# Performance work log

Measured on AMD Instinct MI355X. Metric: run time of the kernel, lower is better.

Reference implementation:

```python
import jax, jax.numpy as jnp
import numpy as np

GAMMA = 0.1   # sdtw_gamma from train_config
WARP = 1.0    # sdtw_warp from train_config
BIG = 1e8     # stand-in for +inf in the DP table (safe in fp32 logsumexp)


def soft_dtw(D, gamma, warp):
    """SoftDTW with warp penalty via anti-diagonal wavefront DP.

    D: [B, N, M] pairwise cost matrix. Returns [B] soft-DTW values.
    Recurrence: R[i,j] = D[i,j] + softmin_gamma(R[i-1,j-1], R[i-1,j]+warp, R[i,j-1]+warp)
    """
    B, N, M = D.shape
    R = jnp.full((B, N + 1, M + 1), BIG, D.dtype)
    R = R.at[:, 0, 0].set(0.0)
    ii = jnp.arange(N)  # cell row indices on a diagonal

    def body(R, k):
        jj = k - ii                       # cell col indices, i+j = k
        valid = (jj >= 0) & (jj < M)
        jc = jnp.clip(jj, 0, M - 1)
        # padded-coordinate predecessors of cell (ii, jj)
        r_diag = R[:, ii, jc]             # R[i-1, j-1]
        r_up = R[:, ii, jc + 1] + warp    # R[i-1, j] + warp
        r_left = R[:, ii + 1, jc] + warp  # R[i, j-1] + warp
        stacked = jnp.stack([r_diag, r_up, r_left], axis=0)  # [3, B, N]
        smin = -gamma * jax.nn.logsumexp(-stacked / gamma, axis=0)
        new = D[:, ii, jc] + smin
        cur = R[:, ii + 1, jc + 1]
        upd = jnp.where(valid[None, :], new, cur)
        # row indices ii+1 are all distinct -> no scatter collisions
        R = R.at[:, ii + 1, jc + 1].set(upd)
        return R, None

    R, _ = jax.lax.scan(body, R, jnp.arange(N + M - 1))
    return R[:, N, M]


def setup_inputs() -> dict:
    key = jax.random.key(0)
    k1, k2, k3, k4 = jax.random.split(key, 4)
    mel_pred = jax.random.normal(k1, (4, 512, 80), dtype=jnp.float32)
    mel_target = jax.random.normal(k2, (4, 512, 80), dtype=jnp.float32)
    log_d_pred = jax.random.normal(k3, (4, 128), dtype=jnp.float32)
    d_target = jax.random.randint(k4, (4, 128), 0, 20)
    return {"mel_pred": mel_pred, "mel_target": mel_target,
            "log_d_pred": log_d_pred, "d_target": d_target}


def reference(mel_pred, mel_target, log_d_pred, d_target):
    B, T, _ = mel_pred.shape
    # pairwise L1 frame distance: D[b,i,j] = sum_m |pred[b,i,m] - tgt[b,j,m]|
    D = jnp.abs(mel_pred[:, :, None, :] - mel_target[:, None, :, :]).sum(-1)
    sdtw = soft_dtw(D, GAMMA, WARP)           # [B]
    mel_loss = (sdtw / T).mean()
    # L1 (reduction='none' -> mean) on log-durations
    log_d_target = jnp.log(d_target.astype(jnp.float32) + 1.0)
    duration_loss = jnp.abs(log_d_pred - log_d_target).mean()
    return mel_loss + duration_loss
```

## Files before the change

kernel.cpp:

```cpp
#include <hip/hip_runtime.h>
#include <hip/hip_bf16.h>
#include <hip/hip_fp16.h>
#include <math.h>

#define BIGF 1e8f
#define BIGS 28672.0f

__device__ inline float min3f(float a, float b, float c) {
    float d;
    asm("v_min3_f32 %0, %1, %2, %3" : "=v"(d) : "v"(a), "v"(b), "v"(c));
    return d;
}
__device__ inline float addh_lo(unsigned pw, float c) {
    float d;
    asm("v_fma_mix_f32 %0, %1, 1.0, %2 op_sel:[0,0,0] op_sel_hi:[1,0,0]"
        : "=v"(d) : "v"(pw), "v"(c));
    return d;
}
__device__ inline float addh_hi(unsigned pw, float c) {
    float d;
    asm("v_fma_mix_f32 %0, %1, 1.0, %2 op_sel:[1,0,0] op_sel_hi:[1,0,0]"
        : "=v"(d) : "v"(pw), "v"(c));
    return d;
}

__global__ __launch_bounds__(256) void prep_kernel(
        const float* __restrict__ pred, const float* __restrict__ targ,
        __half* __restrict__ Dh) {
    const int bid = blockIdx.x;
    const int t   = threadIdx.x;

    if (bid < 256) {
        const int b  = bid >> 6;
        const int i0 = ((bid >> 3) & 7) * 64;
        const int j0 = (bid & 7) * 64;
        __shared__ float sp[64][81];
        __shared__ float st[64][81];

        const float4* __restrict__ p4 = (const float4*)(pred + ((size_t)b * 512 + i0) * 80);
        const float4* __restrict__ t4 = (const float4*)(targ + ((size_t)b * 512 + j0) * 80);
        #pragma unroll
        for (int q = 0; q < 5; ++q) {
            int idx = q * 256 + t;
            int r = idx / 20, dq = idx % 20;
            float4 v = p4[r * 20 + dq];
            sp[r][dq*4+0]=v.x; sp[r][dq*4+1]=v.y; sp[r][dq*4+2]=v.z; sp[r][dq*4+3]=v.w;
            float4 w = t4[r * 20 + dq];
            st[r][dq*4+0]=w.x; st[r][dq*4+1]=w.y; st[r][dq*4+2]=w.z; st[r][dq*4+3]=w.w;
        }
        __syncthreads();

        const int tx = t & 15, ty = t >> 4;
        float acc[4][4];
        #pragma unroll
        for (int r = 0; r < 4; ++r)
            #pragma unroll
            for (int c = 0; c < 4; ++c) acc[r][c] = 0.f;

        #pragma unroll 4
        for (int d = 0; d < 80; ++d) {
            float a0 = sp[4*ty+0][d], a1 = sp[4*ty+1][d], a2 = sp[4*ty+2][d], a3 = sp[4*ty+3][d];
            float b0 = st[4*tx+0][d], b1 = st[4*tx+1][d], b2 = st[4*tx+2][d], b3 = st[4*tx+3][d];
            acc[0][0] += fabsf(a0-b0); acc[0][1] += fabsf(a0-b1); acc[0][2] += fabsf(a0-b2); acc[0][3] += fabsf(a0-b3);
            acc[1][0] += fabsf(a1-b0); acc[1][1] += fabsf(a1-b1); acc[1][2] += fabsf(a1-b2); acc[1][3] += fabsf(a1-b3);
            acc[2][0] += fabsf(a2-b0); acc[2][1] += fabsf(a2-b1); acc[2][2] += fabsf(a2-b2); acc[2][3] += fabsf(a2-b3);
            acc[3][0] += fabsf(a3-b0); acc[3][1] += fabsf(a3-b1); acc[3][2] += fabsf(a3-b2); acc[3][3] += fabsf(a3-b3);
        }

        #pragma unroll
        for (int r = 0; r < 4; ++r) {
            #pragma unroll
            for (int c = 0; c < 4; ++c) {
                int i = i0 + 4*ty + r;
                int j = j0 + 4*tx + c;
                float v = acc[r][c];
                float w = ((i | j) == 0) ? v : (v + 2.0f);
                Dh[((size_t)b * 1023 + (i + j)) * 512 + i] = __float2half(w);
            }
        }
    } else {
        const int k  = bid - 256;
        const int lo = (k > 511) ? (k - 511) : 0;
        const int hi = (k < 511) ? k : 511;
        const __half big = __float2half(BIGS);
        #pragma unroll
        for (int b = 0; b < 4; ++b) {
            __half* row = Dh + ((size_t)b * 1023 + k) * 512;
            int i1 = t;
            int i2 = t + 256;
            if (i1 < lo || i1 > hi) row[i1] = big;
            if (i2 < lo || i2 > hi) row[i2] = big;
        }
    }
}

#define DPPSHR(x) __int_as_float(__builtin_amdgcn_update_dpp(                 \
        __float_as_int(BIGF), __float_as_int(x), 0x138, 0xF, 0xF, false))

#define STEP(V1, V2, Q)                                                       \
  {                                                                           \
    float nb1 = DPPSHR(V1[7]);                                                \
    float nb2 = DPPSHR(V2[7]);                                                \
    V2[7] = addh_hi(Q.w, min3f(V2[6], V1[6], V1[7]));                         \
    V2[6] = addh_lo(Q.w, min3f(V2[5], V1[5], V1[6]));                         \
    V2[5] = addh_hi(Q.z, min3f(V2[4], V1[4], V1[5]));                         \
    V2[4] = addh_lo(Q.z, min3f(V2[3], V1[3], V1[4]));                         \
    V2[3] = addh_hi(Q.y, min3f(V2[2], V1[2], V1[3]));                         \
    V2[2] = addh_lo(Q.y, min3f(V2[1], V1[1], V1[2]));                         \
    V2[1] = addh_hi(Q.x, min3f(V2[0], V1[0], V1[1]));                         \
    V2[0] = addh_lo(Q.x, min3f(nb2,   nb1,   V1[0]));                         \
  }

__global__ __launch_bounds__(128, 1) void dp_kernel(
        const __half* __restrict__ Dh,
        const float* __restrict__ ldp, const int* __restrict__ dt,
        float* __restrict__ out) {
    const int tid = threadIdx.x;
    if (tid >= 64) {
        if (blockIdx.x == 0) {
            const int l = tid - 64;
            float s = 0.f;
            #pragma unroll
            for (int q = 0; q < 8; ++q) {
                int idx = l * 8 + q;
                s += fabsf(ldp[idx] - logf((float)dt[idx] + 1.0f));
            }
            #pragma unroll
            for (int o = 32; o > 0; o >>= 1) s += __shfl_down(s, o);
            if (l == 0) atomicAdd(out, s * (1.0f / 512.0f));
        }
        return;
    }

    const int b    = blockIdx.x;
    const int lane = tid;
    const char* __restrict__ base = (const char*)(Dh + (size_t)b * 1023 * 512);

    float A[8], B[8];
    #pragma unroll
    for (int r = 0; r < 8; ++r) { A[r] = BIGF; B[r] = BIGF; }

    {
        float c00 = __half2float(*(const __half*)base);
        B[0] = (lane == 0) ? c00 : BIGF;
    }
    __builtin_amdgcn_sched_barrier(0);

    unsigned voff = (unsigned)lane * 16u + 1024u;
    uint4 P[32];
    #pragma unroll
    for (int p = 0; p < 32; ++p) {
        asm volatile("global_load_dwordx4 %0, %1, %2"
                     : "=v"(P[p]) : "v"(voff), "s"(base) : "memory");
        voff += 1024u;
    }

    for (int t = 0; t < 31; ++t) {
#define PH(p, Vx, Vy)                                                         \
        asm volatile("s_waitcnt vmcnt(31)" ::: "memory");                     \
        __builtin_amdgcn_sched_barrier(0);                                    \
        STEP(Vx, Vy, P[p])                                                    \
        asm volatile("global_load_dwordx4 %0, %1, %2"                         \
                     : "=v"(P[p]) : "v"(voff), "s"(base) : "memory");         \
        voff += 1024u;
        PH(0,B,A)   PH(1,A,B)   PH(2,B,A)   PH(3,A,B)
        PH(4,B,A)   PH(5,A,B)   PH(6,B,A)   PH(7,A,B)
        PH(8,B,A)   PH(9,A,B)   PH(10,B,A)  PH(11,A,B)
        PH(12,B,A)  PH(13,A,B)  PH(14,B,A)  PH(15,A,B)
        PH(16,B,A)  PH(17,A,B)  PH(18,B,A)  PH(19,A,B)
        PH(20,B,A)  PH(21,A,B)  PH(22,B,A)  PH(23,A,B)
        PH(24,B,A)  PH(25,A,B)  PH(26,B,A)  PH(27,A,B)
        PH(28,B,A)  PH(29,A,B)  PH(30,B,A)  PH(31,A,B)
#undef PH
    }

    asm volatile("s_waitcnt vmcnt(0)" ::: "memory");
    __builtin_amdgcn_sched_barrier(0);
    STEP(B,A,P[0])   STEP(A,B,P[1])   STEP(B,A,P[2])   STEP(A,B,P[3])
    STEP(B,A,P[4])   STEP(A,B,P[5])   STEP(B,A,P[6])   STEP(A,B,P[7])
    STEP(B,A,P[8])   STEP(A,B,P[9])   STEP(B,A,P[10])  STEP(A,B,P[11])
    STEP(B,A,P[12])  STEP(A,B,P[13])  STEP(B,A,P[14])  STEP(A,B,P[15])
    STEP(B,A,P[16])  STEP(A,B,P[17])  STEP(B,A,P[18])  STEP(A,B,P[19])
    STEP(B,A,P[20])  STEP(A,B,P[21])  STEP(B,A,P[22])  STEP(A,B,P[23])
    STEP(B,A,P[24])  STEP(A,B,P[25])  STEP(B,A,P[26])  STEP(A,B,P[27])
    STEP(B,A,P[28])  STEP(A,B,P[29])

    if (lane == 63) atomicAdd(out, (B[7] - 1022.0f) * (1.0f / 2048.0f));
}

extern "C" void kernel_launch(void* const* d_in, const int* in_sizes, int n_in,
                              void* d_out, int out_size, void* d_ws, size_t ws_size,
                              hipStream_t stream) {
    const float* pred = (const float*)d_in[0];
    const float* targ = (const float*)d_in[1];
    const float* ldp  = (const float*)d_in[2];
    const int*   dt   = (const int*)d_in[3];
    float* out = (float*)d_out;

    __half* Dh = (__half*)d_ws;

    hipMemsetAsync(out, 0, sizeof(float), stream);
    prep_kernel<<<256 + 1023, 256, 0, stream>>>(pred, targ, Dh);
    dp_kernel<<<4, 128, 0, stream>>>(Dh, ldp, dt, out);
}
```

Baseline: 73.12 us.

## Stream DP cost diagonals through LDS with global_load_lds ring buffer

Replaces the 32-register prefetch ring of global loads in the DP kernel with direct global-to-LDS DMA into a 32-slot shared-memory ring. Values are read back from LDS four steps ahead into a small set of registers. The goal is to free VGPRs and cut register pressure while keeping the deep prefetch that hides memory latency on the serial wavefront loop. It adds LDS read latency and relies on vmcnt accounting for the LDS DMA, which is delicate to get right.

```diff
diff --git a/kernel.cpp b/kernel.cpp
--- a/kernel.cpp
+++ b/kernel.cpp
@@ -22,6 +22,12 @@
     asm("v_fma_mix_f32 %0, %1, 1.0, %2 op_sel:[1,0,0] op_sel_hi:[1,0,0]"
         : "=v"(d) : "v"(pw), "v"(c));
     return d;
+}
+
+__device__ __forceinline__ void dma16(const void* g,
+        __attribute__((address_space(3))) unsigned int* l) {
+    __builtin_amdgcn_global_load_lds(
+        (const __attribute__((address_space(1))) unsigned int*)g, l, 16, 0, 0);
 }
 
 __global__ __launch_bounds__(256) void prep_kernel(
@@ -115,6 +121,7 @@
         const __half* __restrict__ Dh,
         const float* __restrict__ ldp, const int* __restrict__ dt,
         float* __restrict__ out) {
+    __shared__ alignas(16) unsigned char smem[32 * 1024];
     const int tid = threadIdx.x;
     if (tid >= 64) {
         if (blockIdx.x == 0) {
@@ -134,56 +141,68 @@
 
     const int b    = blockIdx.x;
     const int lane = tid;
-    const char* __restrict__ base = (const char*)(Dh + (size_t)b * 1023 * 512);
+    const char* __restrict__ gb = (const char*)(Dh + (size_t)b * 1023 * 512);
+    const unsigned laneoff = (unsigned)lane * 16u;
+    const unsigned smoff   = (unsigned)(uintptr_t)&smem[0];
+
+#define S3(slot) ((__attribute__((address_space(3))) unsigned int*)(smoff + (unsigned)(slot) * 1024u))
+#define QREAD(slot) (*(const uint4*)(smem + (unsigned)(slot) * 1024u + laneoff))
 
     float A[8], B[8];
     #pragma unroll
     for (int r = 0; r < 8; ++r) { A[r] = BIGF; B[r] = BIGF; }
 
     {
-        float c00 = __half2float(*(const __half*)base);
+        float c00 = __half2float(*(const __half*)gb);
         B[0] = (lane == 0) ? c00 : BIGF;
     }
-    __builtin_amdgcn_sched_barrier(0);
-
-    unsigned voff = (unsigned)lane * 16u + 1024u;
-    uint4 P[32];
+    asm volatile("" :: "v"(B[0]));
+    asm volatile("s_waitcnt vmcnt(0)" ::: "memory");
+
+    unsigned voff = laneoff + 1024u;
     #pragma unroll
-    for (int p = 0; p < 32; ++p) {
-        asm volatile("global_load_dwordx4 %0, %1, %2"
-                     : "=v"(P[p]) : "v"(voff), "s"(base) : "memory");
+    for (int d = 1; d <= 32; ++d) {
+        dma16(gb + voff, S3(d & 31));
         voff += 1024u;
     }
+    asm volatile("s_waitcnt vmcnt(29)" ::: "memory");
+    uint4 Q0 = QREAD(1);
+    uint4 Q1 = QREAD(2);
+    uint4 Q2 = QREAD(3);
+    uint4 Q3;
 
     for (int t = 0; t < 31; ++t) {
-#define PH(p, Vx, Vy)                                                         \
-        asm volatile("s_waitcnt vmcnt(31)" ::: "memory");                     \
-        __builtin_amdgcn_sched_barrier(0);                                    \
-        STEP(Vx, Vy, P[p])                                                    \
-        asm volatile("global_load_dwordx4 %0, %1, %2"                         \
-                     : "=v"(P[p]) : "v"(voff), "s"(base) : "memory");         \
+#define PH(p, Vx, Vy, Qc, Qn)                                                 \
+        asm volatile("s_waitcnt vmcnt(28)" ::: "memory");                     \
+        Qn = QREAD(((p) + 4) & 31);                                           \
+        STEP(Vx, Vy, Qc)                                                      \
+        dma16(gb + voff, S3(((p) + 1) & 31));                                 \
         voff += 1024u;
-        PH(0,B,A)   PH(1,A,B)   PH(2,B,A)   PH(3,A,B)
-        PH(4,B,A)   PH(5,A,B)   PH(6,B,A)   PH(7,A,B)
-        PH(8,B,A)   PH(9,A,B)   PH(10,B,A)  PH(11,A,B)
-        PH(12,B,A)  PH(13,A,B)  PH(14,B,A)  PH(15,A,B)
-        PH(16,B,A)  PH(17,A,B)  PH(18,B,A)  PH(19,A,B)
-        PH(20,B,A)  PH(21,A,B)  PH(22,B,A)  PH(23,A,B)
-        PH(24,B,A)  PH(25,A,B)  PH(26,B,A)  PH(27,A,B)
-        PH(28,B,A)  PH(29,A,B)  PH(30,B,A)  PH(31,A,B)
+#define PH4(p0)                                                               \
+        PH(p0 + 0, B, A, Q0, Q3)                                              \
+        PH(p0 + 1, A, B, Q1, Q0)                                              \
+        PH(p0 + 2, B, A, Q2, Q1)                                              \
+        PH(p0 + 3, A, B, Q3, Q2)
+        PH4(0) PH4(4) PH4(8) PH4(12) PH4(16) PH4(20) PH4(24) PH4(28)
+#undef PH4
 #undef PH
     }
 
     asm volatile("s_waitcnt vmcnt(0)" ::: "memory");
-    __builtin_amdgcn_sched_barrier(0);
-    STEP(B,A,P[0])   STEP(A,B,P[1])   STEP(B,A,P[2])   STEP(A,B,P[3])
-    STEP(B,A,P[4])   STEP(A,B,P[5])   STEP(B,A,P[6])   STEP(A,B,P[7])
-    STEP(B,A,P[8])   STEP(A,B,P[9])   STEP(B,A,P[10])  STEP(A,B,P[11])
-    STEP(B,A,P[12])  STEP(A,B,P[13])  STEP(B,A,P[14])  STEP(A,B,P[15])
-    STEP(B,A,P[16])  STEP(A,B,P[17])  STEP(B,A,P[18])  STEP(A,B,P[19])
-    STEP(B,A,P[20])  STEP(A,B,P[21])  STEP(B,A,P[22])  STEP(A,B,P[23])
-    STEP(B,A,P[24])  STEP(A,B,P[25])  STEP(B,A,P[26])  STEP(A,B,P[27])
-    STEP(B,A,P[28])  STEP(A,B,P[29])
+#define TP(p, Vx, Vy, Qc, Qn)                                                 \
+        Qn = QREAD(((p) + 4) & 31);                                           \
+        STEP(Vx, Vy, Qc)
+    TP(0,B,A,Q0,Q3)  TP(1,A,B,Q1,Q0)  TP(2,B,A,Q2,Q1)  TP(3,A,B,Q3,Q2)
+    TP(4,B,A,Q0,Q3)  TP(5,A,B,Q1,Q0)  TP(6,B,A,Q2,Q1)  TP(7,A,B,Q3,Q2)
+    TP(8,B,A,Q0,Q3)  TP(9,A,B,Q1,Q0)  TP(10,B,A,Q2,Q1) TP(11,A,B,Q3,Q2)
+    TP(12,B,A,Q0,Q3) TP(13,A,B,Q1,Q0) TP(14,B,A,Q2,Q1) TP(15,A,B,Q3,Q2)
+    TP(16,B,A,Q0,Q3) TP(17,A,B,Q1,Q0) TP(18,B,A,Q2,Q1) TP(19,A,B,Q3,Q2)
+    TP(20,B,A,Q0,Q3) TP(21,A,B,Q1,Q0) TP(22,B,A,Q2,Q1) TP(23,A,B,Q3,Q2)
+    TP(24,B,A,Q0,Q3) TP(25,A,B,Q1,Q0) TP(26,B,A,Q2,Q1)
+    STEP(A,B,Q3)
+    STEP(B,A,Q0)
+    STEP(A,B,Q1)
+#undef TP
 
     if (lane == 63) atomicAdd(out, (B[7] - 1022.0f) * (1.0f / 2048.0f));
 }
```

Measured after the change: 257.8 us. +252.6%, slower.
